# Optimization experiments

Measured on AMD Instinct MI355X. Metric: run time of the kernel, lower is better.

## Reference

```python
import jax, jax.numpy as jnp
import numpy as np

B, E, H, NE, K, P, IMG, NC, FF, DEPTH = 64, 256, 8, 4, 2, 16, 224, 38, 1024, 4
S = (IMG // P) ** 2 + 1  # 197 tokens (cls + patches)


def layernorm(x, w, b, eps=1e-5):
    m = x.mean(-1, keepdims=True)
    v = ((x - m) ** 2).mean(-1, keepdims=True)
    return (x - m) / jnp.sqrt(v + eps) * w + b


def forward(x, conv_w, conv_b, cls_token, pos_embed, ln1_w, ln1_b, qkv_w, qkv_b,
            out_w, out_b, ln2_w, ln2_b, router_w, router_b, e_w1, e_b1, e_w2, e_b2,
            norm_w, norm_b, h1_w, h1_b, h2_w, h2_b):
    Bn = x.shape[0]
    dh = E // H
    # patch embedding: conv stride=kernel=P
    z = jax.lax.conv_general_dilated(x, conv_w, (P, P), 'VALID',
                                     dimension_numbers=('NCHW', 'OIHW', 'NCHW'))
    z = z + conv_b[None, :, None, None]
    z = z.reshape(Bn, E, -1).transpose(0, 2, 1)  # [B, 196, E]
    z = jnp.concatenate([jnp.broadcast_to(cls_token, (Bn, 1, E)), z], axis=1) + pos_embed
    for i in range(DEPTH):
        # --- multi-head self-attention ---
        h = layernorm(z, ln1_w[i], ln1_b[i])
        qkv = h @ qkv_w[i] + qkv_b[i]                       # [B,S,3E]
        q, k, v = jnp.split(qkv, 3, axis=-1)
        q = q.reshape(Bn, -1, H, dh)
        k = k.reshape(Bn, -1, H, dh)
        v = v.reshape(Bn, -1, H, dh)
        att = jax.nn.softmax(jnp.einsum('bqhd,bkhd->bhqk', q, k) / jnp.sqrt(jnp.float32(dh)), axis=-1)
        ctx = jnp.einsum('bhqk,bkhd->bqhd', att, v).reshape(Bn, -1, E)
        z = z + ctx @ out_w[i] + out_b[i]
        # --- MoE FFN (top-k routing; expert sum expressed densely via gate weights) ---
        xf = layernorm(z, ln2_w[i], ln2_b[i]).reshape(-1, E)  # [T,E]
        probs = jax.nn.softmax(xf @ router_w[i] + router_b[i], axis=-1)  # [T,NE]
        wk, idx = jax.lax.top_k(probs, K)
        wk = wk / wk.sum(-1, keepdims=True)
        gate = (jax.nn.one_hot(idx, NE, dtype=wk.dtype) * wk[..., None]).sum(1)  # [T,NE]
        he = jax.nn.gelu(jnp.einsum('td,ndh->tnh', xf, e_w1[i]) + e_b1[i], approximate=False)
        oe = jnp.einsum('tnh,nhd->tnd', he, e_w2[i]) + e_b2[i]
        z = z + jnp.einsum('tnd,tn->td', oe, gate).reshape(Bn, -1, E)
    cls = layernorm(z[:, 0], norm_w, norm_b)
    h = jax.nn.gelu(cls @ h1_w + h1_b, approximate=False)
    return h @ h2_w + h2_b  # [B, NC]


def setup_inputs() -> dict:
    key = jax.random.key(0)
    ks = jax.random.split(key, 12)
    s = jnp.float32(0.02)
    return {
        'x': jax.random.normal(ks[0], (B, 3, IMG, IMG), jnp.float32),
        'conv_w': jax.random.normal(ks[1], (E, 3, P, P), jnp.float32) * s,
        'conv_b': jnp.zeros((E,), jnp.float32),
        'cls_token': jax.random.normal(ks[2], (1, 1, E), jnp.float32) * s,
        'pos_embed': jax.random.normal(ks[3], (1, S, E), jnp.float32) * s,
        'ln1_w': jnp.ones((DEPTH, E), jnp.float32), 'ln1_b': jnp.zeros((DEPTH, E), jnp.float32),
        'qkv_w': jax.random.normal(ks[4], (DEPTH, E, 3 * E), jnp.float32) * s,
        'qkv_b': jnp.zeros((DEPTH, 3 * E), jnp.float32),
        'out_w': jax.random.normal(ks[5], (DEPTH, E, E), jnp.float32) * s,
        'out_b': jnp.zeros((DEPTH, E), jnp.float32),
        'ln2_w': jnp.ones((DEPTH, E), jnp.float32), 'ln2_b': jnp.zeros((DEPTH, E), jnp.float32),
        'router_w': jax.random.normal(ks[6], (DEPTH, E, NE), jnp.float32) * s,
        'router_b': jnp.zeros((DEPTH, NE), jnp.float32),
        'e_w1': jax.random.normal(ks[7], (DEPTH, NE, E, FF), jnp.float32) * s,
        'e_b1': jnp.zeros((DEPTH, NE, FF), jnp.float32),
        'e_w2': jax.random.normal(ks[8], (DEPTH, NE, FF, E), jnp.float32) * s,
        'e_b2': jnp.zeros((DEPTH, NE, E), jnp.float32),
        'norm_w': jnp.ones((E,), jnp.float32), 'norm_b': jnp.zeros((E,), jnp.float32),
        'h1_w': jax.random.normal(ks[9], (E, E), jnp.float32) * s,
        'h1_b': jnp.zeros((E,), jnp.float32),
        'h2_w': jax.random.normal(ks[10], (E, NC), jnp.float32) * s,
        'h2_b': jnp.zeros((NC,), jnp.float32),
    }


def reference(x, conv_w, conv_b, cls_token, pos_embed, ln1_w, ln1_b, qkv_w, qkv_b,
              out_w, out_b, ln2_w, ln2_b, router_w, router_b, e_w1, e_b1, e_w2, e_b2,
              norm_w, norm_b, h1_w, h1_b, h2_w, h2_b):
    return forward(x, conv_w, conv_b, cls_token, pos_embed, ln1_w, ln1_b, qkv_w, qkv_b,
                   out_w, out_b, ln2_w, ln2_b, router_w, router_b, e_w1, e_b1, e_w2, e_b2,
                   norm_w, norm_b, h1_w, h1_b, h2_w, h2_b)
```

## Files before the change

### kernel.cpp

```cpp
#include <hip/hip_runtime.h>
#include <hip/hip_bf16.h>

#define T_TOK 12608
#define MPAD  12672
#define S_TOK 197
#define DEPTH_L 4

typedef __attribute__((ext_vector_type(8))) short short8;
typedef __attribute__((ext_vector_type(4))) short short4v;
typedef __attribute__((ext_vector_type(4))) float f32x4;

using gvoid = __attribute__((address_space(1))) const void;
using lvoid = __attribute__((address_space(3))) void;

__device__ __forceinline__ float gelu_f(float x) {
    return 0.5f * x * (1.f + erff(x * 0.70710678118654752440f));
}

__device__ __forceinline__ void split2(float v, __hip_bfloat16& h, __hip_bfloat16& l) {
    h = __float2bfloat16(v);
    l = __float2bfloat16(v - __bfloat162float(h));
}

template<int MODE>
__global__ __launch_bounds__(256, 4)
void gemm3(const short* __restrict__ Ahi, const short* __restrict__ Alo, int ldA,
           const short* __restrict__ Bext,
           float* __restrict__ outf, __hip_bfloat16* __restrict__ outh, int ldOut,
           const float* __restrict__ bias, const float* __restrict__ gate,
           const float* __restrict__ aux,
           const int* __restrict__ rowmap, const int* __restrict__ cntp,
           const int* __restrict__ basep,
           int Mvalid, int N, int K, int npanels)
{
    __shared__ short As[128 * 64];
    __shared__ short Bs[128 * 64];
    const int tid  = threadIdx.x;
    const int wid  = tid >> 6;
    const int lane = tid & 63;

    const int xcd = blockIdx.x & 7;
    const int j   = blockIdx.x >> 3;
    const int p   = (j % 13) * 8 + xcd;
    const int c   = j / 13;
    if (p >= npanels) return;
    const int row0 = p * 128;
    const int col0 = c * 128;

    const int wr = (wid >> 1) * 64;
    const int wc = (wid & 1) * 64;
    const int e  = (MODE == 2 || MODE == 3) ? blockIdx.z : 0;

    int Mv = Mvalid;
    int baseRow = 0;
    const int* rmap = nullptr;
    if (MODE == 2 || MODE == 3) {
        Mv = cntp[e];
        if (row0 >= Mv) return;
        baseRow = basep[e];
        if (MODE == 2) rmap = rowmap + e * T_TOK;
    }

    int arow[4];
    if (MODE == 2) {
#pragma unroll
        for (int i = 0; i < 4; ++i) {
            int gr = row0 + (i * 4 + wid) * 8 + (lane >> 3);
            if (gr > Mv - 1) gr = Mv - 1;
            arow[i] = rmap[gr];
        }
    }

    f32x4 acc[4][4];
#pragma unroll
    for (int m = 0; m < 4; ++m)
#pragma unroll
        for (int n = 0; n < 4; ++n) acc[m][n] = (f32x4){0.f, 0.f, 0.f, 0.f};

    const int ld3 = 3 * K;
    const size_t strideA = (size_t)ldA * 2;
    const size_t strideB = (size_t)ld3 * 2;
    const char* Bbase = (const char*)Bext + ((size_t)e * N + col0) * strideB;

    for (int k0 = 0; k0 < ld3; k0 += 64) {
        const int regio = (k0 >= K) + (k0 >= 2 * K);
        const short* Asrc = (regio == 1) ? Alo : Ahi;
        const int ka = k0 - regio * K;
        __syncthreads();
#pragma unroll
        for (int i = 0; i < 4; ++i) {
            const int chunk = (i * 4 + wid) * 1024;
            const int off = chunk + lane * 16;
            const int r = off >> 7;
            const int cb = off & 127;
            const int cbs = cb ^ ((r & 7) << 4);
            const char* asrc;
            if (MODE == 2) {
                asrc = (const char*)Asrc + (size_t)arow[i] * strideA + (size_t)ka * 2 + cbs;
            } else {
                asrc = (const char*)Asrc + (size_t)(baseRow + row0 + r) * strideA + (size_t)ka * 2 + cbs;
            }
            __builtin_amdgcn_global_load_lds((gvoid*)asrc, (lvoid*)((char*)As + chunk), 16, 0, 0);
            __builtin_amdgcn_global_load_lds(
                (gvoid*)(Bbase + (size_t)r * strideB + (size_t)k0 * 2 + cbs),
                (lvoid*)((char*)Bs + chunk), 16, 0, 0);
        }
        __syncthreads();

        const int lr = lane & 15;
        const int kbB = (lane >> 4) * 16;
#pragma unroll
        for (int kk = 0; kk < 2; ++kk) {
            short8 af[4], bfr[4];
#pragma unroll
            for (int m = 0; m < 4; ++m) {
                const int row = wr + m * 16 + lr;
                const int cbb = (kk * 64 + kbB) ^ ((row & 7) << 4);
                af[m] = *(const short8*)((const char*)As + row * 128 + cbb);
            }
#pragma unroll
            for (int n = 0; n < 4; ++n) {
                const int row = wc + n * 16 + lr;
                const int cbb = (kk * 64 + kbB) ^ ((row & 7) << 4);
                bfr[n] = *(const short8*)((const char*)Bs + row * 128 + cbb);
            }
#pragma unroll
            for (int m = 0; m < 4; ++m)
#pragma unroll
                for (int n = 0; n < 4; ++n)
                    acc[m][n] = __builtin_amdgcn_mfma_f32_16x16x32_bf16(af[m], bfr[n], acc[m][n], 0, 0, 0);
        }
    }

    const int lr = lane & 15;
    const int rb4 = (lane >> 4) * 4;
#pragma unroll
    for (int m = 0; m < 4; ++m) {
#pragma unroll
        for (int n = 0; n < 4; ++n) {
#pragma unroll
            for (int r = 0; r < 4; ++r) {
                const int row = row0 + wr + m * 16 + rb4 + r;
                const int col = col0 + wc + n * 16 + lr;
                if (row >= Mv) continue;
                const float v = acc[m][n][r];
                if (MODE == 0) {
                    outf[(size_t)row * N + col] = v + bias[col];
                } else if (MODE == 1) {
                    outf[(size_t)row * N + col] += v + bias[col];
                } else if (MODE == 2) {
                    const float g = gate[rmap[row] * 4 + e];
                    const float y = g * gelu_f(v + bias[e * N + col]);
                    __hip_bfloat16 h, l; split2(y, h, l);
                    outh[((size_t)(baseRow + row)) * ldOut + col] = h;
                    outh[((size_t)(baseRow + row)) * ldOut + N + col] = l;
                } else if (MODE == 3) {
                    outf[((size_t)(baseRow + row)) * N + col] = v;
                } else if (MODE == 4) {
                    const int bi = row / 196;
                    const int pp = row - bi * 196;
                    outf[((size_t)(bi * 197 + 1 + pp)) * N + col] = v + bias[col] + aux[(size_t)(1 + pp) * N + col];
                }
            }
        }
    }
}

__global__ void ln_split(const float* __restrict__ x, const float* __restrict__ w,
                         const float* __restrict__ b, __hip_bfloat16* __restrict__ hi,
                         __hip_bfloat16* __restrict__ lo, float* __restrict__ out32,
                         int nrows, int in_stride)
{
    const int row = blockIdx.x * 4 + (threadIdx.x >> 6);
    const int lane = threadIdx.x & 63;
    if (row >= nrows) return;
    const float4 v = ((const float4*)(x + (size_t)row * in_stride))[lane];
    float s = v.x + v.y + v.z + v.w;
#pragma unroll
    for (int o = 32; o; o >>= 1) s += __shfl_xor(s, o);
    const float mean = s * (1.f / 256.f);
    const float dx = v.x - mean, dy = v.y - mean, dz = v.z - mean, dw = v.w - mean;
    float q = dx * dx + dy * dy + dz * dz + dw * dw;
#pragma unroll
    for (int o = 32; o; o >>= 1) q += __shfl_xor(q, o);
    const float inv = rsqrtf(q * (1.f / 256.f) + 1e-5f);
    const int c = lane * 4;
    const float4 wv = ((const float4*)w)[lane];
    const float4 bv = ((const float4*)b)[lane];
    float y[4];
    y[0] = dx * inv * wv.x + bv.x;
    y[1] = dy * inv * wv.y + bv.y;
    y[2] = dz * inv * wv.z + bv.z;
    y[3] = dw * inv * wv.w + bv.w;
    if (hi) {
#pragma unroll
        for (int j = 0; j < 4; ++j) {
            __hip_bfloat16 h, l; split2(y[j], h, l);
            hi[(size_t)row * 256 + c + j] = h;
            lo[(size_t)row * 256 + c + j] = l;
        }
    }
    if (out32) {
        ((float4*)(out32 + (size_t)row * 256))[lane] = make_float4(y[0], y[1], y[2], y[3]);
    }
}

__global__ void ln2_router(const float* __restrict__ x, const float* __restrict__ w,
                           const float* __restrict__ b, __hip_bfloat16* __restrict__ hi,
                           __hip_bfloat16* __restrict__ lo,
                           const float* __restrict__ rw, const float* __restrict__ rb,
                           float* __restrict__ gate, int* __restrict__ top2,
                           int* __restrict__ cnt, int T)
{
    if (blockIdx.x == 0 && threadIdx.x < 4) cnt[threadIdx.x] = 0;
    const int row = blockIdx.x * 4 + (threadIdx.x >> 6);
    const int lane = threadIdx.x & 63;
    if (row >= T) return;
    const float4 v = ((const float4*)(x + (size_t)row * 256))[lane];
    float s = v.x + v.y + v.z + v.w;
#pragma unroll
    for (int o = 32; o; o >>= 1) s += __shfl_xor(s, o);
    const float mean = s * (1.f / 256.f);
    const float dx = v.x - mean, dy = v.y - mean, dz = v.z - mean, dw = v.w - mean;
    float q = dx * dx + dy * dy + dz * dz + dw * dw;
#pragma unroll
    for (int o = 32; o; o >>= 1) q += __shfl_xor(q, o);
    const float inv = rsqrtf(q * (1.f / 256.f) + 1e-5f);
    const int c = lane * 4;
    const float4 wv = ((const float4*)w)[lane];
    const float4 bv = ((const float4*)b)[lane];
    float y[4];
    y[0] = dx * inv * wv.x + bv.x;
    y[1] = dy * inv * wv.y + bv.y;
    y[2] = dz * inv * wv.z + bv.z;
    y[3] = dw * inv * wv.w + bv.w;
#pragma unroll
    for (int jj = 0; jj < 4; ++jj) {
        __hip_bfloat16 h, l; split2(y[jj], h, l);
        hi[(size_t)row * 256 + c + jj] = h;
        lo[(size_t)row * 256 + c + jj] = l;
    }
    float a0 = 0, a1 = 0, a2 = 0, a3 = 0;
#pragma unroll
    for (int jj = 0; jj < 4; ++jj) {
        const float xs = y[jj];
        const float4 wr4 = ((const float4*)rw)[lane * 4 + jj];
        a0 += xs * wr4.x; a1 += xs * wr4.y; a2 += xs * wr4.z; a3 += xs * wr4.w;
    }
#pragma unroll
    for (int o = 32; o; o >>= 1) {
        a0 += __shfl_xor(a0, o); a1 += __shfl_xor(a1, o);
        a2 += __shfl_xor(a2, o); a3 += __shfl_xor(a3, o);
    }
    if (lane == 0) {
        float l[4] = {a0 + rb[0], a1 + rb[1], a2 + rb[2], a3 + rb[3]};
        const float m = fmaxf(fmaxf(l[0], l[1]), fmaxf(l[2], l[3]));
        float pr[4]; float sm = 0.f;
#pragma unroll
        for (int n = 0; n < 4; ++n) { pr[n] = expf(l[n] - m); sm += pr[n]; }
#pragma unroll
        for (int n = 0; n < 4; ++n) pr[n] /= sm;
        int i0 = 0;
        for (int n = 1; n < 4; ++n) if (pr[n] > pr[i0]) i0 = n;
        int i1 = -1;
        for (int n = 0; n < 4; ++n) { if (n == i0) continue; if (i1 < 0 || pr[n] > pr[i1]) i1 = n; }
        const float wsum = pr[i0] + pr[i1];
        float g[4] = {0.f, 0.f, 0.f, 0.f};
        g[i0] = pr[i0] / wsum; g[i1] = pr[i1] / wsum;
        ((float4*)gate)[row] = make_float4(g[0], g[1], g[2], g[3]);
        top2[row] = i0 | (i1 << 4);
    }
}

__global__ void build_list(const int* __restrict__ top2, int* __restrict__ cnt,
                           int* __restrict__ list, int* __restrict__ poslist, int T)
{
    const int t = blockIdx.x * 256 + threadIdx.x;
    const int lane = threadIdx.x & 63;
    int i0 = -1, i1 = -1;
    if (t < T) { const int v = top2[t]; i0 = v & 15; i1 = v >> 4; }
    const unsigned long long lt = (lane == 63) ? ~0ull >> 1 : (1ull << lane) - 1;
#pragma unroll
    for (int e = 0; e < 4; ++e) {
#pragma unroll
        for (int s = 0; s < 2; ++s) {
            const int sel = s ? i1 : i0;
            const unsigned long long m = __ballot(sel == e);
            if (m) {
                const int leader = __ffsll((long long)m) - 1;
                int base = 0;
                if (lane == leader) base = atomicAdd(&cnt[e], __popcll(m));
                base = __shfl(base, leader);
                if (sel == e) {
                    const int p = base + __popcll(m & lt);
                    list[e * T_TOK + p] = t;
                    poslist[2 * t + s] = p;
                }
            }
        }
    }
}

__global__ void calc_base(const int* __restrict__ cnt, int* __restrict__ base)
{
    if (threadIdx.x == 0) {
        int s = 0;
#pragma unroll
        for (int e = 0; e < 4; ++e) { base[e] = s; s += cnt[e]; }
    }
}

__global__ void combine_ln(const float* __restrict__ ebuf, const int* __restrict__ top2,
                           const int* __restrict__ poslist, const int* __restrict__ basep,
                           const float* __restrict__ gate, const float* __restrict__ e_b2,
                           float* __restrict__ z,
                           const float* __restrict__ lnw, const float* __restrict__ lnb,
                           __hip_bfloat16* __restrict__ hi, __hip_bfloat16* __restrict__ lo,
                           int T)
{
    const int t = blockIdx.x * 4 + (threadIdx.x >> 6);
    const int lane = threadIdx.x & 63;
    if (t >= T) return;
    const int tp = top2[t];
    const int e0 = tp & 15, e1 = tp >> 4;
    const size_t g0 = (size_t)basep[e0] + poslist[2 * t];
    const size_t g1 = (size_t)basep[e1] + poslist[2 * t + 1];
    const float4 a  = ((const float4*)(ebuf + g0 * 256))[lane];
    const float4 bq = ((const float4*)(ebuf + g1 * 256))[lane];
    const float4 gw = ((const float4*)gate)[t];
    const float4 b0 = ((const float4*)(e_b2 + 0 * 256))[lane];
    const float4 b1 = ((const float4*)(e_b2 + 1 * 256))[lane];
    const float4 b2 = ((const float4*)(e_b2 + 2 * 256))[lane];
    const float4 b3 = ((const float4*)(e_b2 + 3 * 256))[lane];
    float4* zp = (float4*)(z + (size_t)t * 256);
    float4 acc = zp[lane];
    acc.x += a.x + bq.x + gw.x * b0.x + gw.y * b1.x + gw.z * b2.x + gw.w * b3.x;
    acc.y += a.y + bq.y + gw.x * b0.y + gw.y * b1.y + gw.z * b2.y + gw.w * b3.y;
    acc.z += a.z + bq.z + gw.x * b0.z + gw.y * b1.z + gw.z * b2.z + gw.w * b3.z;
    acc.w += a.w + bq.w + gw.x * b0.w + gw.y * b1.w + gw.z * b2.w + gw.w * b3.w;
    zp[lane] = acc;
    if (lnw) {
        float s = acc.x + acc.y + acc.z + acc.w;
#pragma unroll
        for (int o = 32; o; o >>= 1) s += __shfl_xor(s, o);
        const float mean = s * (1.f / 256.f);
        const float dx = acc.x - mean, dy = acc.y - mean, dz = acc.z - mean, dw = acc.w - mean;
        float q = dx * dx + dy * dy + dz * dz + dw * dw;
#pragma unroll
        for (int o = 32; o; o >>= 1) q += __shfl_xor(q, o);
        const float inv = rsqrtf(q * (1.f / 256.f) + 1e-5f);
        const int c = lane * 4;
        const float4 wv = ((const float4*)lnw)[lane];
        const float4 bv = ((const float4*)lnb)[lane];
        float y[4];
        y[0] = dx * inv * wv.x + bv.x;
        y[1] = dy * inv * wv.y + bv.y;
        y[2] = dz * inv * wv.z + bv.z;
        y[3] = dw * inv * wv.w + bv.w;
#pragma unroll
        for (int jj = 0; jj < 4; ++jj) {
            __hip_bfloat16 h, l; split2(y[jj], h, l);
            hi[(size_t)t * 256 + c + jj] = h;
            lo[(size_t)t * 256 + c + jj] = l;
        }
    }
}

#define VSTR 232
__global__ __launch_bounds__(256, 1)
void attn_v6(const float* __restrict__ qkv, __hip_bfloat16* __restrict__ ctxhi,
             __hip_bfloat16* __restrict__ ctxlo)
{
    __shared__ short Qhf[13 * 512], Qlf[13 * 512], Khf[13 * 512], Klf[13 * 512];
    __shared__ short Vth[32 * VSTR], Vtl[32 * VSTR];
    __shared__ short Pfh[4 * 512], Pfl[4 * 512];
    const int b = blockIdx.x >> 3;
    const int h = blockIdx.x & 7;
    const int tid = threadIdx.x, lane = tid & 63, wid = tid >> 6;
    const int g = lane >> 4;
    const size_t base = ((size_t)b * S_TOK) * 768 + h * 32;

    for (int idx = tid; idx < 208 * 8; idx += 256) {
        const int s = idx >> 3, c4 = idx & 7;
        float4 qv = make_float4(0.f, 0.f, 0.f, 0.f);
        float4 kv = make_float4(0.f, 0.f, 0.f, 0.f);
        if (s < S_TOK) {
            const float* row = qkv + base + (size_t)s * 768;
            qv = *(const float4*)(row + c4 * 4);
            kv = *(const float4*)(row + 256 + c4 * 4);
        }
        short4v qh, ql, kh, kl;
#pragma unroll
        for (int j = 0; j < 4; ++j) {
            __hip_bfloat16 hh, ll;
            split2((&qv.x)[j], hh, ll);
            qh[j] = *reinterpret_cast<short*>(&hh); ql[j] = *reinterpret_cast<short*>(&ll);
            split2((&kv.x)[j], hh, ll);
            kh[j] = *reinterpret_cast<short*>(&hh); kl[j] = *reinterpret_cast<short*>(&ll);
        }
        const int off = (s >> 4) * 512 + ((s & 15) + ((c4 >> 1) << 4)) * 8 + (c4 & 1) * 4;
        *(short4v*)&Qhf[off] = qh; *(short4v*)&Qlf[off] = ql;
        *(short4v*)&Khf[off] = kh; *(short4v*)&Klf[off] = kl;
    }
    for (int idx = tid; idx < S_TOK * 8; idx += 256) {
        const int s = idx >> 3, c4 = idx & 7;
        const float4 vv = *(const float4*)(qkv + base + (size_t)s * 768 + 512 + c4 * 4);
#pragma unroll
        for (int j = 0; j < 4; ++j) {
            __hip_bfloat16 hh, ll; split2((&vv.x)[j], hh, ll);
            Vth[(c4 * 4 + j) * VSTR + s] = *reinterpret_cast<short*>(&hh);
            Vtl[(c4 * 4 + j) * VSTR + s] = *reinterpret_cast<short*>(&ll);
        }
    }
    for (int idx = tid; idx < 32 * (VSTR - S_TOK); idx += 256) {
        const int d = idx / (VSTR - S_TOK), s = S_TOK + idx % (VSTR - S_TOK);
        Vth[d * VSTR + s] = 0;
        Vtl[d * VSTR + s] = 0;
    }
    __syncthreads();

    const float scale = 0.17677669529663687f;
    for (int qt = wid; qt < 13; qt += 4) {
        const short8 qh  = *(const short8*)&Qhf[qt * 512 + lane * 8];
        const short8 qlo = *(const short8*)&Qlf[qt * 512 + lane * 8];
        f32x4 o0 = (f32x4){0.f, 0.f, 0.f, 0.f};
        f32x4 o1 = (f32x4){0.f, 0.f, 0.f, 0.f};
        float lsum = 0.f;
        for (int kp = 0; kp < 7; ++kp) {
#pragma unroll
            for (int half = 0; half < 2; ++half) {
                const int kt = kp * 2 + half;
                short4v pkh = (short4v){0, 0, 0, 0};
                short4v pkl = (short4v){0, 0, 0, 0};
                if (kt < 13) {
                    const short8 kh = *(const short8*)&Khf[kt * 512 + lane * 8];
                    const short8 kl = *(const short8*)&Klf[kt * 512 + lane * 8];
                    f32x4 st = (f32x4){0.f, 0.f, 0.f, 0.f};
                    st = __builtin_amdgcn_mfma_f32_16x16x32_bf16(kh, qh,  st, 0, 0, 0);
                    st = __builtin_amdgcn_mfma_f32_16x16x32_bf16(kl, qh,  st, 0, 0, 0);
                    st = __builtin_amdgcn_mfma_f32_16x16x32_bf16(kh, qlo, st, 0, 0, 0);
#pragma unroll
                    for (int r = 0; r < 4; ++r) {
                        const int sg = kt * 16 + g * 4 + r;
                        const float e = (sg < S_TOK) ? __expf(st[r] * scale) : 0.f;
                        lsum += e;
                        __hip_bfloat16 hh, ll; split2(e, hh, ll);
                        pkh[r] = *reinterpret_cast<short*>(&hh);
                        pkl[r] = *reinterpret_cast<short*>(&ll);
                    }
                }
                const int slb = half * 16 + g * 4;
                const int lp = (lane & 15) + ((slb >> 3) << 4);
                *(short4v*)&Pfh[wid * 512 + lp * 8 + (slb & 4)] = pkh;
                *(short4v*)&Pfl[wid * 512 + lp * 8 + (slb & 4)] = pkl;
            }
            asm volatile("s_waitcnt lgkmcnt(0)" ::: "memory");
            __builtin_amdgcn_sched_barrier(0);
            const short8 pfh = *(const short8*)&Pfh[wid * 512 + lane * 8];
            const short8 pfl = *(const short8*)&Pfl[wid * 512 + lane * 8];
            const int vo = kp * 32 + g * 8;
            const short8 vah = *(const short8*)&Vth[(lane & 15) * VSTR + vo];
            const short8 valo = *(const short8*)&Vtl[(lane & 15) * VSTR + vo];
            const short8 vbh = *(const short8*)&Vth[((lane & 15) + 16) * VSTR + vo];
            const short8 vblo = *(const short8*)&Vtl[((lane & 15) + 16) * VSTR + vo];
            o0 = __builtin_amdgcn_mfma_f32_16x16x32_bf16(vah,  pfh, o0, 0, 0, 0);
            o0 = __builtin_amdgcn_mfma_f32_16x16x32_bf16(vah,  pfl, o0, 0, 0, 0);
            o0 = __builtin_amdgcn_mfma_f32_16x16x32_bf16(valo, pfh, o0, 0, 0, 0);
            o1 = __builtin_amdgcn_mfma_f32_16x16x32_bf16(vbh,  pfh, o1, 0, 0, 0);
            o1 = __builtin_amdgcn_mfma_f32_16x16x32_bf16(vbh,  pfl, o1, 0, 0, 0);
            o1 = __builtin_amdgcn_mfma_f32_16x16x32_bf16(vblo, pfh, o1, 0, 0, 0);
        }
        float lr = lsum;
        lr += __shfl_xor(lr, 16);
        lr += __shfl_xor(lr, 32);
        const int q = qt * 16 + (lane & 15);
        if (q < S_TOK) {
            const float inv = 1.f / lr;
            const size_t orow = ((size_t)b * S_TOK + q) * 256 + h * 32;
#pragma unroll
            for (int r = 0; r < 4; ++r) {
                __hip_bfloat16 hh, ll;
                split2(o0[r] * inv, hh, ll);
                ctxhi[orow + g * 4 + r] = hh;
                ctxlo[orow + g * 4 + r] = ll;
                split2(o1[r] * inv, hh, ll);
                ctxhi[orow + 16 + g * 4 + r] = hh;
                ctxlo[orow + 16 + g * 4 + r] = ll;
            }
        }
    }
}

__global__ void transpose_split(const float* __restrict__ in, short* __restrict__ out,
                                int K, int N, size_t inBatch, size_t outBatch)
{
    __shared__ float tile[32][33];
    const int n0 = blockIdx.x * 32, k0 = blockIdx.y * 32;
    const float* src = in + blockIdx.z * inBatch;
    __hip_bfloat16* dst = (__hip_bfloat16*)out + blockIdx.z * outBatch;
    const int tx = threadIdx.x & 31, ty = threadIdx.x >> 5;
#pragma unroll
    for (int i = 0; i < 32; i += 8)
        tile[ty + i][tx] = src[(size_t)(k0 + ty + i) * N + (n0 + tx)];
    __syncthreads();
    const int ld3 = 3 * K;
#pragma unroll
    for (int i = 0; i < 32; i += 8) {
        const float v = tile[tx][ty + i];
        __hip_bfloat16 h, l; split2(v, h, l);
        const int n = n0 + ty + i, k = k0 + tx;
        dst[(size_t)n * ld3 + k] = h;
        dst[(size_t)n * ld3 + K + k] = h;
        dst[(size_t)n * ld3 + 2 * K + k] = l;
    }
}

__global__ void split_rows(const float* __restrict__ in, short* __restrict__ out, int N, int K)
{
    const int idx = blockIdx.x * 256 + threadIdx.x;
    if (idx >= N * K) return;
    const int n = idx / K, k = idx - n * K;
    __hip_bfloat16 h, l; split2(in[idx], h, l);
    __hip_bfloat16* dst = (__hip_bfloat16*)out;
    dst[(size_t)n * 3 * K + k] = h;
    dst[(size_t)n * 3 * K + K + k] = h;
    dst[(size_t)n * 3 * K + 2 * K + k] = l;
}

__global__ void im2col_split(const float* __restrict__ x, short* __restrict__ out)
{
    const int t = blockIdx.x;
    const int b = t / 196, p = t - b * 196;
    const int py = p / 14, px = p - py * 14;
    __hip_bfloat16* dst = (__hip_bfloat16*)out;
    for (int c_ = threadIdx.x; c_ < 768; c_ += 256) {
        const int c = c_ >> 8, r = c_ & 255;
        const int ky = r >> 4, kx = r & 15;
        const float v = x[(((size_t)b * 3 + c) * 224 + (py * 16 + ky)) * 224 + (px * 16 + kx)];
        __hip_bfloat16 h, l; split2(v, h, l);
        dst[(size_t)t * 1536 + c_] = h;
        dst[(size_t)t * 1536 + 768 + c_] = l;
    }
}

__global__ void cls_init(const float* __restrict__ cls_tok, const float* __restrict__ pos,
                         float* __restrict__ z)
{
    const int b = blockIdx.x, e = threadIdx.x;
    z[((size_t)b * S_TOK) * 256 + e] = cls_tok[e] + pos[e];
}

__global__ void head1_kernel(const float* __restrict__ clsln, const float* __restrict__ w,
                             const float* __restrict__ bias, float* __restrict__ hbuf)
{
    __shared__ float xs[256];
    const int b = blockIdx.x, n = threadIdx.x;
    xs[n] = clsln[b * 256 + n];
    __syncthreads();
    float acc = bias[n];
    for (int k = 0; k < 256; ++k) acc += xs[k] * w[k * 256 + n];
    hbuf[b * 256 + n] = gelu_f(acc);
}

__global__ void head2_kernel(const float* __restrict__ hbuf, const float* __restrict__ w,
                             const float* __restrict__ bias, float* __restrict__ out)
{
    __shared__ float xs[256];
    const int b = blockIdx.x, t = threadIdx.x;
    xs[t] = hbuf[b * 256 + t];
    __syncthreads();
    if (t < 38) {
        float acc = bias[t];
        for (int k = 0; k < 256; ++k) acc += xs[k] * w[k * 38 + t];
        out[b * 38 + t] = acc;
    }
}

extern "C" void kernel_launch(void* const* d_in, const int* in_sizes, int n_in,
                              void* d_out, int out_size, void* d_ws, size_t ws_size,
                              hipStream_t stream)
{
    const float* x       = (const float*)d_in[0];
    const float* conv_w  = (const float*)d_in[1];
    const float* conv_b  = (const float*)d_in[2];
    const float* cls_tok = (const float*)d_in[3];
    const float* pos     = (const float*)d_in[4];
    const float* ln1_w   = (const float*)d_in[5];
    const float* ln1_b   = (const float*)d_in[6];
    const float* qkv_w   = (const float*)d_in[7];
    const float* qkv_b   = (const float*)d_in[8];
    const float* out_w   = (const float*)d_in[9];
    const float* out_b   = (const float*)d_in[10];
    const float* ln2_w   = (const float*)d_in[11];
    const float* ln2_b   = (const float*)d_in[12];
    const float* rw      = (const float*)d_in[13];
    const float* rb      = (const float*)d_in[14];
    const float* e_w1    = (const float*)d_in[15];
    const float* e_b1    = (const float*)d_in[16];
    const float* e_w2    = (const float*)d_in[17];
    const float* e_b2    = (const float*)d_in[18];
    const float* norm_w  = (const float*)d_in[19];
    const float* norm_b  = (const float*)d_in[20];
    const float* h1_w    = (const float*)d_in[21];
    const float* h1_b    = (const float*)d_in[22];
    const float* h2_w    = (const float*)d_in[23];
    const float* h2_b    = (const float*)d_in[24];
    float* outp = (float*)d_out;

    char* ws = (char*)d_ws;
    size_t off = 0;
    auto alloc = [&](size_t bytes) -> char* {
        char* p = ws + off;
        off += (bytes + 255) & ~(size_t)255;
        return p;
    };

    float* zbuf    = (float*)alloc((size_t)T_TOK * 256 * 4);
    short* xfhi    = (short*)alloc((size_t)MPAD * 256 * 2);
    short* xflo    = (short*)alloc((size_t)MPAD * 256 * 2);
    float* qkvbuf  = (float*)alloc((size_t)T_TOK * 768 * 4);
    float* ebuf    = qkvbuf;
    short* ctxhi   = (short*)alloc((size_t)MPAD * 256 * 2);
    short* ctxlo   = (short*)alloc((size_t)MPAD * 256 * 2);
    float* gate    = (float*)alloc((size_t)T_TOK * 4 * 4);
    short* he_full = (short*)alloc((size_t)(2 * MPAD) * 2048 * 2);
    short* patches = he_full;
    short* qkvWext = (short*)alloc((size_t)768 * 768 * 2);
    short* woutext = (short*)alloc((size_t)256 * 768 * 2);
    short* w1ext   = (short*)alloc((size_t)4 * 1024 * 768 * 2);
    short* w2ext   = (short*)alloc((size_t)4 * 256 * 3072 * 2);
    short* convext = (short*)alloc((size_t)256 * 2304 * 2);
    float* clsln   = (float*)alloc((size_t)64 * 256 * 4);
    float* hbuf    = (float*)alloc((size_t)64 * 256 * 4);
    int*   elist   = (int*)alloc((size_t)4 * T_TOK * 4);
    int*   poslist = (int*)alloc((size_t)2 * T_TOK * 4);
    int*   ecnt    = (int*)alloc(256);
    int*   ebase   = (int*)alloc(256);
    int*   top2    = (int*)alloc((size_t)T_TOK * 4);

    split_rows<<<768, 256, 0, stream>>>(conv_w, convext, 256, 768);
    im2col_split<<<12544, 256, 0, stream>>>(x, patches);
    gemm3<4><<<208, 256, 0, stream>>>(patches, patches + 768, 1536, convext,
                                      zbuf, nullptr, 0, conv_b, nullptr, pos,
                                      nullptr, nullptr, nullptr, 12544, 256, 768, 98);
    cls_init<<<64, 256, 0, stream>>>(cls_tok, pos, zbuf);

    ln_split<<<3152, 256, 0, stream>>>(zbuf, ln1_w, ln1_b,
                                       (__hip_bfloat16*)xfhi, (__hip_bfloat16*)xflo,
                                       nullptr, T_TOK, 256);

    for (int i = 0; i < DEPTH_L; ++i) {
        transpose_split<<<dim3(24, 8, 1), 256, 0, stream>>>(qkv_w + (size_t)i * 196608, qkvWext,
                                                            256, 768, 0, 0);
        gemm3<0><<<624, 256, 0, stream>>>(xfhi, xflo, 256, qkvWext,
                                          qkvbuf, nullptr, 0, qkv_b + i * 768,
                                          nullptr, nullptr, nullptr, nullptr, nullptr,
                                          T_TOK, 768, 256, 99);
        attn_v6<<<512, 256, 0, stream>>>(qkvbuf, (__hip_bfloat16*)ctxhi, (__hip_bfloat16*)ctxlo);
        transpose_split<<<dim3(8, 8, 1), 256, 0, stream>>>(out_w + (size_t)i * 65536, woutext,
                                                           256, 256, 0, 0);
        gemm3<1><<<208, 256, 0, stream>>>(ctxhi, ctxlo, 256, woutext,
                                          zbuf, nullptr, 0, out_b + i * 256,
                                          nullptr, nullptr, nullptr, nullptr, nullptr,
                                          T_TOK, 256, 256, 99);
        ln2_router<<<3152, 256, 0, stream>>>(zbuf, ln2_w + i * 256, ln2_b + i * 256,
                                             (__hip_bfloat16*)xfhi, (__hip_bfloat16*)xflo,
                                             rw + i * 1024, rb + i * 4, gate, top2, ecnt, T_TOK);
        build_list<<<50, 256, 0, stream>>>(top2, ecnt, elist, poslist, T_TOK);
        calc_base<<<1, 64, 0, stream>>>(ecnt, ebase);
        transpose_split<<<dim3(32, 8, 4), 256, 0, stream>>>(e_w1 + (size_t)i * 1048576, w1ext,
                                                            256, 1024, 262144, 786432);
        transpose_split<<<dim3(8, 32, 4), 256, 0, stream>>>(e_w2 + (size_t)i * 1048576, w2ext,
                                                            1024, 256, 262144, 786432);
        gemm3<2><<<dim3(832, 1, 4), 256, 0, stream>>>(xfhi, xflo, 256, w1ext,
                                                      nullptr, (__hip_bfloat16*)he_full, 2048,
                                                      e_b1 + (size_t)i * 4096, gate, nullptr,
                                                      elist, ecnt, ebase, T_TOK, 1024, 256, 99);
        gemm3<3><<<dim3(208, 1, 4), 256, 0, stream>>>(he_full, he_full + 1024, 2048, w2ext,
                                                      ebuf, nullptr, 0, nullptr, nullptr, nullptr,
                                                      nullptr, ecnt, ebase, T_TOK, 256, 1024, 99);
        if (i < DEPTH_L - 1) {
            combine_ln<<<3152, 256, 0, stream>>>(ebuf, top2, poslist, ebase, gate,
                                                 e_b2 + (size_t)i * 1024, zbuf,
                                                 ln1_w + (i + 1) * 256, ln1_b + (i + 1) * 256,
                                                 (__hip_bfloat16*)xfhi, (__hip_bfloat16*)xflo,
                                                 T_TOK);
        } else {
            combine_ln<<<3152, 256, 0, stream>>>(ebuf, top2, poslist, ebase, gate,
                                                 e_b2 + (size_t)i * 1024, zbuf,
                                                 nullptr, nullptr, nullptr, nullptr, T_TOK);
        }
    }

    ln_split<<<16, 256, 0, stream>>>(zbuf, norm_w, norm_b, nullptr, nullptr, clsln, 64, S_TOK * 256);
    head1_kernel<<<64, 256, 0, stream>>>(clsln, h1_w, h1_b, hbuf);
    head2_kernel<<<64, 256, 0, stream>>>(hbuf, h2_w, h2_b, outp);

    (void)in_sizes; (void)n_in; (void)out_size; (void)ws_size;
}
```

Before: 1.401 ms.

## Split expert down-projection GEMM along K and sum partials in combine

The second expert GEMM (K = 3*1024 in the hi/lo split scheme) now runs with two K-slices over blockIdx.y. Each slice writes its partial sums to a separate buffer, and combine_ln adds the two partials. The goal is more blocks in flight for this under-occupied GEMM and a shorter K loop per block. The cost is an extra partial buffer, more memory traffic and extra loads in combine. Launch bounds are also raised from 4 to 5 waves-per-SIMD occupancy, which may increase register pressure.

```diff
diff --git a/kernel.cpp b/kernel.cpp
--- a/kernel.cpp
+++ b/kernel.cpp
@@ -23,7 +23,7 @@
 }
 
 template<int MODE>
-__global__ __launch_bounds__(256, 4)
+__global__ __launch_bounds__(256, 5)
 void gemm3(const short* __restrict__ Ahi, const short* __restrict__ Alo, int ldA,
            const short* __restrict__ Bext,
            float* __restrict__ outf, __hip_bfloat16* __restrict__ outh, int ldOut,
@@ -31,7 +31,7 @@
            const float* __restrict__ aux,
            const int* __restrict__ rowmap, const int* __restrict__ cntp,
            const int* __restrict__ basep,
-           int Mvalid, int N, int K, int npanels)
+           int Mvalid, int N, int K, int npanels, int kChunk, size_t outStride)
 {
     __shared__ short As[128 * 64];
     __shared__ short Bs[128 * 64];
@@ -82,7 +82,10 @@
     const size_t strideB = (size_t)ld3 * 2;
     const char* Bbase = (const char*)Bext + ((size_t)e * N + col0) * strideB;
 
-    for (int k0 = 0; k0 < ld3; k0 += 64) {
+    const int kBeg = blockIdx.y * kChunk;
+    int kEnd = kBeg + kChunk; if (kEnd > ld3) kEnd = ld3;
+
+    for (int k0 = kBeg; k0 < kEnd; k0 += 64) {
         const int regio = (k0 >= K) + (k0 >= 2 * K);
         const short* Asrc = (regio == 1) ? Alo : Ahi;
         const int ka = k0 - regio * K;
@@ -155,7 +158,7 @@
                     outh[((size_t)(baseRow + row)) * ldOut + col] = h;
                     outh[((size_t)(baseRow + row)) * ldOut + N + col] = l;
                 } else if (MODE == 3) {
-                    outf[((size_t)(baseRow + row)) * N + col] = v;
+                    outf[outStride * blockIdx.y + ((size_t)(baseRow + row)) * N + col] = v;
                 } else if (MODE == 4) {
                     const int bi = row / 196;
                     const int pp = row - bi * 196;
@@ -310,7 +313,8 @@
     }
 }
 
-__global__ void combine_ln(const float* __restrict__ ebuf, const int* __restrict__ top2,
+__global__ void combine_ln(const float* __restrict__ ebuf, size_t sliceOff,
+                           const int* __restrict__ top2,
                            const int* __restrict__ poslist, const int* __restrict__ basep,
                            const float* __restrict__ gate, const float* __restrict__ e_b2,
                            float* __restrict__ z,
@@ -327,6 +331,8 @@
     const size_t g1 = (size_t)basep[e1] + poslist[2 * t + 1];
     const float4 a  = ((const float4*)(ebuf + g0 * 256))[lane];
     const float4 bq = ((const float4*)(ebuf + g1 * 256))[lane];
+    const float4 a2 = ((const float4*)(ebuf + sliceOff + g0 * 256))[lane];
+    const float4 b2q = ((const float4*)(ebuf + sliceOff + g1 * 256))[lane];
     const float4 gw = ((const float4*)gate)[t];
     const float4 b0 = ((const float4*)(e_b2 + 0 * 256))[lane];
     const float4 b1 = ((const float4*)(e_b2 + 1 * 256))[lane];
@@ -334,10 +340,10 @@
     const float4 b3 = ((const float4*)(e_b2 + 3 * 256))[lane];
     float4* zp = (float4*)(z + (size_t)t * 256);
     float4 acc = zp[lane];
-    acc.x += a.x + bq.x + gw.x * b0.x + gw.y * b1.x + gw.z * b2.x + gw.w * b3.x;
-    acc.y += a.y + bq.y + gw.x * b0.y + gw.y * b1.y + gw.z * b2.y + gw.w * b3.y;
-    acc.z += a.z + bq.z + gw.x * b0.z + gw.y * b1.z + gw.z * b2.z + gw.w * b3.z;
-    acc.w += a.w + bq.w + gw.x * b0.w + gw.y * b1.w + gw.z * b2.w + gw.w * b3.w;
+    acc.x += (a.x + a2.x) + (bq.x + b2q.x) + gw.x * b0.x + gw.y * b1.x + gw.z * b2.x + gw.w * b3.x;
+    acc.y += (a.y + a2.y) + (bq.y + b2q.y) + gw.x * b0.y + gw.y * b1.y + gw.z * b2.y + gw.w * b3.y;
+    acc.z += (a.z + a2.z) + (bq.z + b2q.z) + gw.x * b0.z + gw.y * b1.z + gw.z * b2.z + gw.w * b3.z;
+    acc.w += (a.w + a2.w) + (bq.w + b2q.w) + gw.x * b0.w + gw.y * b1.w + gw.z * b2.w + gw.w * b3.w;
     zp[lane] = acc;
     if (lnw) {
         float s = acc.x + acc.y + acc.z + acc.w;
@@ -620,6 +626,7 @@
     short* xflo    = (short*)alloc((size_t)MPAD * 256 * 2);
     float* qkvbuf  = (float*)alloc((size_t)T_TOK * 768 * 4);
     float* ebuf    = qkvbuf;
+    float* ebuf1   = (float*)alloc((size_t)(2 * T_TOK) * 256 * 4);
     short* ctxhi   = (short*)alloc((size_t)MPAD * 256 * 2);
     short* ctxlo   = (short*)alloc((size_t)MPAD * 256 * 2);
     float* gate    = (float*)alloc((size_t)T_TOK * 4 * 4);
@@ -638,11 +645,14 @@
     int*   ebase   = (int*)alloc(256);
     int*   top2    = (int*)alloc((size_t)T_TOK * 4);
 
+    const size_t sliceOff = (size_t)(ebuf1 - ebuf);
+
     split_rows<<<768, 256, 0, stream>>>(conv_w, convext, 256, 768);
     im2col_split<<<12544, 256, 0, stream>>>(x, patches);
     gemm3<4><<<208, 256, 0, stream>>>(patches, patches + 768, 1536, convext,
                                       zbuf, nullptr, 0, conv_b, nullptr, pos,
-                                      nullptr, nullptr, nullptr, 12544, 256, 768, 98);
+                                      nullptr, nullptr, nullptr, 12544, 256, 768, 98,
+                                      3 * 768, 0);
     cls_init<<<64, 256, 0, stream>>>(cls_tok, pos, zbuf);
 
     ln_split<<<3152, 256, 0, stream>>>(zbuf, ln1_w, ln1_b,
@@ -655,14 +665,14 @@
         gemm3<0><<<624, 256, 0, stream>>>(xfhi, xflo, 256, qkvWext,
                                           qkvbuf, nullptr, 0, qkv_b + i * 768,
                                           nullptr, nullptr, nullptr, nullptr, nullptr,
-                                          T_TOK, 768, 256, 99);
+                                          T_TOK, 768, 256, 99, 3 * 256, 0);
         attn_v6<<<512, 256, 0, stream>>>(qkvbuf, (__hip_bfloat16*)ctxhi, (__hip_bfloat16*)ctxlo);
         transpose_split<<<dim3(8, 8, 1), 256, 0, stream>>>(out_w + (size_t)i * 65536, woutext,
                                                            256, 256, 0, 0);
         gemm3<1><<<208, 256, 0, stream>>>(ctxhi, ctxlo, 256, woutext,
                                           zbuf, nullptr, 0, out_b + i * 256,
                                           nullptr, nullptr, nullptr, nullptr, nullptr,
-                                          T_TOK, 256, 256, 99);
+                                          T_TOK, 256, 256, 99, 3 * 256, 0);
         ln2_router<<<3152, 256, 0, stream>>>(zbuf, ln2_w + i * 256, ln2_b + i * 256,
                                              (__hip_bfloat16*)xfhi, (__hip_bfloat16*)xflo,
                                              rw + i * 1024, rb + i * 4, gate, top2, ecnt, T_TOK);
@@ -675,18 +685,20 @@
         gemm3<2><<<dim3(832, 1, 4), 256, 0, stream>>>(xfhi, xflo, 256, w1ext,
                                                       nullptr, (__hip_bfloat16*)he_full, 2048,
                                                       e_b1 + (size_t)i * 4096, gate, nullptr,
-                                                      elist, ecnt, ebase, T_TOK, 1024, 256, 99);
-        gemm3<3><<<dim3(208, 1, 4), 256, 0, stream>>>(he_full, he_full + 1024, 2048, w2ext,
+                                                      elist, ecnt, ebase, T_TOK, 1024, 256, 99,
+                                                      3 * 256, 0);
+        gemm3<3><<<dim3(208, 2, 4), 256, 0, stream>>>(he_full, he_full + 1024, 2048, w2ext,
                                                       ebuf, nullptr, 0, nullptr, nullptr, nullptr,
-                                                      nullptr, ecnt, ebase, T_TOK, 256, 1024, 99);
+                                                      nullptr, ecnt, ebase, T_TOK, 256, 1024, 99,
+                                                      1536, sliceOff);
         if (i < DEPTH_L - 1) {
-            combine_ln<<<3152, 256, 0, stream>>>(ebuf, top2, poslist, ebase, gate,
+            combine_ln<<<3152, 256, 0, stream>>>(ebuf, sliceOff, top2, poslist, ebase, gate,
                                                  e_b2 + (size_t)i * 1024, zbuf,
                                                  ln1_w + (i + 1) * 256, ln1_b + (i + 1) * 256,
                                                  (__hip_bfloat16*)xfhi, (__hip_bfloat16*)xflo,
                                                  T_TOK);
         } else {
-            combine_ln<<<3152, 256, 0, stream>>>(ebuf, top2, poslist, ebase, gate,
+            combine_ln<<<3152, 256, 0, stream>>>(ebuf, sliceOff, top2, poslist, ebase, gate,
                                                  e_b2 + (size_t)i * 1024, zbuf,
                                                  nullptr, nullptr, nullptr, nullptr, T_TOK);
         }
```

Measured after the change: 1.806 ms. +28.9%, slower.
